# Kernel optimization log

Measured on AMD Instinct MI355X. Metric: run time of the kernel, lower is better.

Reference implementation:

```python
import jax, jax.numpy as jnp
import numpy as np

B, T, F = 512, 1024, 32
LAYER_SIZES = [64, 32]


def _lstm_layer(x_seq, h0, c0, Wih, Whh, bih, bhh):
    """Single-layer LSTM, batch_first x_seq [B,T,in]. PyTorch gate order i,f,g,o."""
    # Precompute input contribution for all timesteps: [B,T,4H]
    xg = jnp.einsum('bti,gi->btg', x_seq, Wih) + bih + bhh

    def step(carry, xg_t):
        h, c = carry
        gates = xg_t + h @ Whh.T  # [B,4H]
        i, f, g, o = jnp.split(gates, 4, axis=-1)
        i = jax.nn.sigmoid(i)
        f = jax.nn.sigmoid(f)
        g = jnp.tanh(g)
        o = jax.nn.sigmoid(o)
        c = f * c + i * g
        h = o * jnp.tanh(c)
        return (h, c), h

    (hT, cT), hs = jax.lax.scan(step, (h0, c0), jnp.swapaxes(xg, 0, 1))
    return jnp.swapaxes(hs, 0, 1), hT, cT  # [B,T,H], [B,H], [B,H]


def setup_inputs() -> dict:
    key = jax.random.key(0)
    ks = jax.random.split(key, 16)
    x = jax.random.normal(ks[0], (B, T, F), dtype=jnp.float32)
    inp = {'x': x}
    in_size = F
    ki = 1
    for li, h in enumerate(LAYER_SIZES):
        scale_ih = 1.0 / np.sqrt(in_size)
        scale_hh = 1.0 / np.sqrt(h)
        inp[f'W_ih{li}'] = jax.random.normal(ks[ki], (4 * h, in_size), dtype=jnp.float32) * scale_ih; ki += 1
        inp[f'W_hh{li}'] = jax.random.normal(ks[ki], (4 * h, h), dtype=jnp.float32) * scale_hh; ki += 1
        inp[f'b_ih{li}'] = jnp.zeros((4 * h,), dtype=jnp.float32)
        inp[f'b_hh{li}'] = jnp.zeros((4 * h,), dtype=jnp.float32)
        in_size = h
    inp['fc_w'] = jax.random.normal(ks[ki], (1, LAYER_SIZES[-1]), dtype=jnp.float32) * (1.0 / np.sqrt(LAYER_SIZES[-1]))
    inp['fc_b'] = jnp.zeros((1,), dtype=jnp.float32)
    return inp


def reference(x, W_ih0, W_hh0, b_ih0, b_hh0, W_ih1, W_hh1, b_ih1, b_hh1, fc_w, fc_b):
    batch = x.shape[0]
    h0 = jnp.zeros((batch, LAYER_SIZES[0]), dtype=x.dtype)
    c0 = jnp.zeros((batch, LAYER_SIZES[0]), dtype=x.dtype)
    h1 = jnp.zeros((batch, LAYER_SIZES[1]), dtype=x.dtype)
    c1 = jnp.zeros((batch, LAYER_SIZES[1]), dtype=x.dtype)

    out0, hT0, cT0 = _lstm_layer(x, h0, c0, W_ih0, W_hh0, b_ih0, b_hh0)
    # dropout_prob = 0.0 -> identity between layers
    out1, hT1, cT1 = _lstm_layer(out0, h1, c1, W_ih1, W_hh1, b_ih1, b_hh1)

    out = out1[:, -1, :] @ fc_w.T + fc_b  # [B,1]
    # apply_clipped_relu = False -> identity final activation
    return out, hT0, cT0, hT1, cT1
```

## Files before the change

kernel.cpp:

```cpp
#include <hip/hip_runtime.h>

#define B_ 512
#define T_ 1024
#define F_ 32
#define H0_ 64
#define H1_ 32
#define ROWS 2
#define NT 512
#define CH 64
#define NCH (T_ / CH)

typedef _Float16 f16x8 __attribute__((ext_vector_type(8)));
typedef _Float16 f16x4 __attribute__((ext_vector_type(4)));
typedef float f32x4 __attribute__((ext_vector_type(4)));

__device__ __forceinline__ float exp2_f(float x) { return __builtin_amdgcn_exp2f(x); }

__device__ __forceinline__ f16x8 cvt8(const float* p) {
    float4 a = *(const float4*)p;
    float4 b = *(const float4*)(p + 4);
    f16x8 o;
    o[0] = (_Float16)a.x; o[1] = (_Float16)a.y; o[2] = (_Float16)a.z; o[3] = (_Float16)a.w;
    o[4] = (_Float16)b.x; o[5] = (_Float16)b.y; o[6] = (_Float16)b.z; o[7] = (_Float16)b.w;
    return o;
}
__device__ __forceinline__ f16x4 cvt4(float4 v) {
    f16x4 o;
    o[0] = (_Float16)v.x; o[1] = (_Float16)v.y; o[2] = (_Float16)v.z; o[3] = (_Float16)v.w;
    return o;
}

#define K_SIG (-1.4426950408889634f)
#define K_TNH (-2.8853900817779268f)

__global__ void __launch_bounds__(NT, 1) lstm2_mfma_kernel(
    const float* __restrict__ x,
    const float* __restrict__ Wih0, const float* __restrict__ Whh0,
    const float* __restrict__ bih0, const float* __restrict__ bhh0,
    const float* __restrict__ Wih1, const float* __restrict__ Whh1,
    const float* __restrict__ bih1, const float* __restrict__ bhh1,
    const float* __restrict__ fcw, const float* __restrict__ fcb,
    float* __restrict__ out)
{
    __shared__ __align__(16) _Float16 xch[2][CH][ROWS][F_];
    __shared__ __align__(16) _Float16 h0b[2][ROWS][H0_];
    __shared__ __align__(16) _Float16 h1b[2][ROWS][H1_];
    __shared__ __align__(16) float wscr[6][128];
    __shared__ float h1fin[ROWS][H1_];

    const int tid = threadIdx.x, blk = blockIdx.x;
    const int wv = tid >> 6, lane = tid & 63;
    const int lrow = lane & 15;
    const int lk   = lane >> 4;
    const bool isL0 = (wv < 4);
    const bool isL1 = (wv == 4 || wv == 5);
    const int U0 = isL0 ? 16 * wv : 16 * (wv - 4);

    f16x8 aw[4][3];
    if (isL0) {
#pragma unroll
        for (int G = 0; G < 4; ++G) {
            const int r = G * H0_ + U0 + lrow;
            aw[G][0] = cvt8(&Wih0[r * F_ + 8 * lk]);
            aw[G][1] = cvt8(&Whh0[r * H0_ + 8 * lk]);
            aw[G][2] = cvt8(&Whh0[r * H0_ + 32 + 8 * lk]);
        }
    } else if (isL1) {
#pragma unroll
        for (int G = 0; G < 4; ++G) {
            const int r = G * H1_ + U0 + lrow;
            aw[G][0] = cvt8(&Wih1[r * H0_ + 8 * lk]);
            aw[G][1] = cvt8(&Wih1[r * H0_ + 32 + 8 * lk]);
            aw[G][2] = cvt8(&Whh1[r * H1_ + 8 * lk]);
        }
    }

    const float kS1 = (lane < 32) ? K_TNH : K_SIG;
    const float kA1 = (lane < 32) ? 2.0f : 1.0f;
    const float kC1 = (lane < 32) ? -1.0f : 0.0f;
    float bK0 = 0.0f, bK1 = 0.0f;
    if (isL0) {
        const int r0 = (lane >> 5) * H0_ + U0 + (lane & 15);
        const int r1 = (2 + (lane >> 5)) * H0_ + U0 + (lane & 15);
        bK0 = (bih0[r0] + bhh0[r0]) * K_SIG;
        bK1 = (bih0[r1] + bhh0[r1]) * kS1;
    } else if (isL1) {
        const int r0 = (lane >> 5) * H1_ + U0 + (lane & 15);
        const int r1 = (2 + (lane >> 5)) * H1_ + U0 + (lane & 15);
        bK0 = (bih1[r0] + bhh1[r0]) * K_SIG;
        bK1 = (bih1[r1] + bhh1[r1]) * kS1;
    }

    {
        const float4* x4 = (const float4*)x;
#pragma unroll
        for (int k = 0; k < 2; ++k) {
            const int i = tid + k * NT;
            const int b = i >> 9, rem = i & 511;
            const int s2 = rem >> 3, f4 = rem & 7;
            float4 v = x4[(size_t)(2 * blk + b) * (T_ * (F_ / 4)) + s2 * (F_ / 4) + f4];
            *(f16x4*)&xch[0][s2][b][f4 * 4] = cvt4(v);
        }
    }
    if (tid < 256) ((_Float16*)h0b)[tid] = (_Float16)0.0f;
    if (tid < 128) ((_Float16*)h1b)[tid] = (_Float16)0.0f;
    __syncthreads();

    int p = 0, cb = 0;
    float c = 0.0f, hreg = 0.0f;
    for (int it = 0; it <= T_; ++it) {
        const int s = it & (CH - 1);
        const bool active = (isL0 && it < T_) || (isL1 && it >= 1);
        if (active) {
            f16x8 b0, b1, b2;
            if (isL0) {
                b0 = *(const f16x8*)&xch[cb][s][lane & 1][8 * lk];
                b1 = *(const f16x8*)&h0b[p][lane & 1][8 * lk];
                b2 = *(const f16x8*)&h0b[p][lane & 1][32 + 8 * lk];
            } else {
                b0 = *(const f16x8*)&h0b[p][lane & 1][8 * lk];
                b1 = *(const f16x8*)&h0b[p][lane & 1][32 + 8 * lk];
                b2 = *(const f16x8*)&h1b[p][lane & 1][8 * lk];
            }
            f32x4 acc[4];
#pragma unroll
            for (int G = 0; G < 4; ++G) {
                f32x4 a = {0.f, 0.f, 0.f, 0.f};
                a = __builtin_amdgcn_mfma_f32_16x16x32_f16(aw[G][0], b0, a, 0, 0, 0);
                a = __builtin_amdgcn_mfma_f32_16x16x32_f16(aw[G][1], b1, a, 0, 0, 0);
                a = __builtin_amdgcn_mfma_f32_16x16x32_f16(aw[G][2], b2, a, 0, 0, 0);
                acc[G] = a;
            }
            if (lrow < 2) {
                float* sp = &wscr[wv][lrow * 16 + lk * 4];
#pragma unroll
                for (int G = 0; G < 4; ++G) {
                    *(float2*)&sp[G * 32]     = make_float2(acc[G][0], acc[G][1]);
                    *(float2*)&sp[G * 32 + 2] = make_float2(acc[G][2], acc[G][3]);
                }
            }
            const float v0 = wscr[wv][lane];
            const float v1 = wscr[wv][64 + lane];
            const float act0 = __builtin_amdgcn_rcpf(1.0f + exp2_f(fmaf(v0, K_SIG, bK0)));
            const float rr1  = __builtin_amdgcn_rcpf(1.0f + exp2_f(fmaf(v1, kS1, bK1)));
            const float act1 = fmaf(kA1, rr1, kC1);
            const float fg = __shfl_xor(act0, 32, 64);
            const float og = __shfl_xor(act1, 32, 64);
            c = fmaf(fg, c, act0 * act1);
            const float thr = __builtin_amdgcn_rcpf(1.0f + exp2_f(c * K_TNH));
            const float thc = fmaf(2.0f, thr, -1.0f);
            hreg = og * thc;
            if (lane < 32) {
                const _Float16 hq = (_Float16)hreg;
                if (isL0) h0b[p ^ 1][lane >> 4][U0 + (lane & 15)] = hq;
                else      h1b[p ^ 1][lane >> 4][U0 + (lane & 15)] = hq;
            }
        }
        if (wv >= 6) {
            if (s == 0 && (it >> 6) < (NCH - 1)) {
                const int tbase = it + CH;
                const float4* x4 = (const float4*)x;
                const int ls = tid - 384;
#pragma unroll
                for (int k = 0; k < 8; ++k) {
                    const int i = ls + k * 128;
                    const int b = i >> 9, rem = i & 511;
                    const int s2 = rem >> 3, f4 = rem & 7;
                    float4 v = x4[(size_t)(2 * blk + b) * (T_ * (F_ / 4)) + (tbase + s2) * (F_ / 4) + f4];
                    *(f16x4*)&xch[cb ^ 1][s2][b][f4 * 4] = cvt4(v);
                }
            }
        }
        __syncthreads();
        p ^= 1;
        if (s == CH - 1) cb ^= 1;
    }

    float* hT0 = out + B_;
    float* cT0 = hT0 + B_ * H0_;
    float* hT1 = cT0 + B_ * H0_;
    float* cT1 = hT1 + B_ * H1_;
    if (isL0 && lane < 32) {
        const int row = 2 * blk + (lane >> 4), unit = U0 + (lane & 15);
        hT0[row * H0_ + unit] = hreg;
        cT0[row * H0_ + unit] = c;
    }
    if (isL1 && lane < 32) {
        const int row = 2 * blk + (lane >> 4), unit = U0 + (lane & 15);
        hT1[row * H1_ + unit] = hreg;
        cT1[row * H1_ + unit] = c;
        h1fin[lane >> 4][unit] = hreg;
    }
    __syncthreads();
    if (wv == 0) {
        const int u = lane & 31, r = lane >> 5;
        float v = h1fin[r][u] * fcw[u];
        v += __shfl_xor(v, 16, 64);
        v += __shfl_xor(v, 8, 64);
        v += __shfl_xor(v, 4, 64);
        v += __shfl_xor(v, 2, 64);
        v += __shfl_xor(v, 1, 64);
        if (u == 0) out[2 * blk + r] = v + fcb[0];
    }
}

extern "C" void kernel_launch(void* const* d_in, const int* in_sizes, int n_in,
                              void* d_out, int out_size, void* d_ws, size_t ws_size,
                              hipStream_t stream) {
    const float* x    = (const float*)d_in[0];
    const float* Wih0 = (const float*)d_in[1];
    const float* Whh0 = (const float*)d_in[2];
    const float* bih0 = (const float*)d_in[3];
    const float* bhh0 = (const float*)d_in[4];
    const float* Wih1 = (const float*)d_in[5];
    const float* Whh1 = (const float*)d_in[6];
    const float* bih1 = (const float*)d_in[7];
    const float* bhh1 = (const float*)d_in[8];
    const float* fcw  = (const float*)d_in[9];
    const float* fcb  = (const float*)d_in[10];

    hipLaunchKernelGGL(lstm2_mfma_kernel, dim3(B_ / ROWS), dim3(NT), 0, stream,
                       x, Wih0, Whh0, bih0, bhh0, Wih1, Whh1, bih1, bhh1,
                       fcw, fcb, (float*)d_out);
}
```

Measured before the change: 683.2 us.

## Swap MFMA operands so gate outputs land in registers, drop LDS scratch

Swaps the A/B operands of the MFMA so each lane holds the pre-activations for its hidden unit across both batch rows directly in accumulator registers. The LSTM cell update then runs entirely in registers, removing the LDS scratch round-trip (wscr writes and reads) and the cross-lane shuffles on the serial per-step critical path. In exchange, each lane computes 10 transcendental activations instead of 5, only 16 lanes do useful work, and the code relies on the accumulator element layout matching batch rows.

```diff
diff --git a/kernel.cpp b/kernel.cpp
--- a/kernel.cpp
+++ b/kernel.cpp
@@ -15,6 +15,7 @@
 typedef float f32x4 __attribute__((ext_vector_type(4)));
 
 __device__ __forceinline__ float exp2_f(float x) { return __builtin_amdgcn_exp2f(x); }
+__device__ __forceinline__ float rcp_f(float x) { return __builtin_amdgcn_rcpf(x); }
 
 __device__ __forceinline__ f16x8 cvt8(const float* p) {
     float4 a = *(const float4*)p;
@@ -45,7 +46,6 @@
     __shared__ __align__(16) _Float16 xch[2][CH][ROWS][F_];
     __shared__ __align__(16) _Float16 h0b[2][ROWS][H0_];
     __shared__ __align__(16) _Float16 h1b[2][ROWS][H1_];
-    __shared__ __align__(16) float wscr[6][128];
     __shared__ float h1fin[ROWS][H1_];
 
     const int tid = threadIdx.x, blk = blockIdx.x;
@@ -75,20 +75,19 @@
         }
     }
 
-    const float kS1 = (lane < 32) ? K_TNH : K_SIG;
-    const float kA1 = (lane < 32) ? 2.0f : 1.0f;
-    const float kC1 = (lane < 32) ? -1.0f : 0.0f;
-    float bK0 = 0.0f, bK1 = 0.0f;
+    float bK[4] = {0.f, 0.f, 0.f, 0.f};
     if (isL0) {
-        const int r0 = (lane >> 5) * H0_ + U0 + (lane & 15);
-        const int r1 = (2 + (lane >> 5)) * H0_ + U0 + (lane & 15);
-        bK0 = (bih0[r0] + bhh0[r0]) * K_SIG;
-        bK1 = (bih0[r1] + bhh0[r1]) * kS1;
+#pragma unroll
+        for (int G = 0; G < 4; ++G) {
+            const int r = G * H0_ + U0 + lrow;
+            bK[G] = (bih0[r] + bhh0[r]) * ((G == 2) ? K_TNH : K_SIG);
+        }
     } else if (isL1) {
-        const int r0 = (lane >> 5) * H1_ + U0 + (lane & 15);
-        const int r1 = (2 + (lane >> 5)) * H1_ + U0 + (lane & 15);
-        bK0 = (bih1[r0] + bhh1[r0]) * K_SIG;
-        bK1 = (bih1[r1] + bhh1[r1]) * kS1;
+#pragma unroll
+        for (int G = 0; G < 4; ++G) {
+            const int r = G * H1_ + U0 + lrow;
+            bK[G] = (bih1[r] + bhh1[r]) * ((G == 2) ? K_TNH : K_SIG);
+        }
     }
 
     {
@@ -107,7 +106,8 @@
     __syncthreads();
 
     int p = 0, cb = 0;
-    float c = 0.0f, hreg = 0.0f;
+    float cc[2] = {0.f, 0.f};
+    float hh[2] = {0.f, 0.f};
     for (int it = 0; it <= T_; ++it) {
         const int s = it & (CH - 1);
         const bool active = (isL0 && it < T_) || (isL1 && it >= 1);
@@ -126,34 +126,29 @@
 #pragma unroll
             for (int G = 0; G < 4; ++G) {
                 f32x4 a = {0.f, 0.f, 0.f, 0.f};
-                a = __builtin_amdgcn_mfma_f32_16x16x32_f16(aw[G][0], b0, a, 0, 0, 0);
-                a = __builtin_amdgcn_mfma_f32_16x16x32_f16(aw[G][1], b1, a, 0, 0, 0);
-                a = __builtin_amdgcn_mfma_f32_16x16x32_f16(aw[G][2], b2, a, 0, 0, 0);
+                a = __builtin_amdgcn_mfma_f32_16x16x32_f16(b0, aw[G][0], a, 0, 0, 0);
+                a = __builtin_amdgcn_mfma_f32_16x16x32_f16(b1, aw[G][1], a, 0, 0, 0);
+                a = __builtin_amdgcn_mfma_f32_16x16x32_f16(b2, aw[G][2], a, 0, 0, 0);
                 acc[G] = a;
             }
-            if (lrow < 2) {
-                float* sp = &wscr[wv][lrow * 16 + lk * 4];
-#pragma unroll
-                for (int G = 0; G < 4; ++G) {
-                    *(float2*)&sp[G * 32]     = make_float2(acc[G][0], acc[G][1]);
-                    *(float2*)&sp[G * 32 + 2] = make_float2(acc[G][2], acc[G][3]);
+#pragma unroll
+            for (int r = 0; r < 2; ++r) {
+                const float gi = rcp_f(1.0f + exp2_f(fmaf(acc[0][r], K_SIG, bK[0])));
+                const float gf = rcp_f(1.0f + exp2_f(fmaf(acc[1][r], K_SIG, bK[1])));
+                const float gg = fmaf(2.0f, rcp_f(1.0f + exp2_f(fmaf(acc[2][r], K_TNH, bK[2]))), -1.0f);
+                const float go = rcp_f(1.0f + exp2_f(fmaf(acc[3][r], K_SIG, bK[3])));
+                cc[r] = fmaf(gf, cc[r], gi * gg);
+                const float th = fmaf(2.0f, rcp_f(1.0f + exp2_f(cc[r] * K_TNH)), -1.0f);
+                hh[r] = go * th;
+            }
+            if (lane < 16) {
+                if (isL0) {
+                    h0b[p ^ 1][0][U0 + lane] = (_Float16)hh[0];
+                    h0b[p ^ 1][1][U0 + lane] = (_Float16)hh[1];
+                } else {
+                    h1b[p ^ 1][0][U0 + lane] = (_Float16)hh[0];
+                    h1b[p ^ 1][1][U0 + lane] = (_Float16)hh[1];
                 }
-            }
-            const float v0 = wscr[wv][lane];
-            const float v1 = wscr[wv][64 + lane];
-            const float act0 = __builtin_amdgcn_rcpf(1.0f + exp2_f(fmaf(v0, K_SIG, bK0)));
-            const float rr1  = __builtin_amdgcn_rcpf(1.0f + exp2_f(fmaf(v1, kS1, bK1)));
-            const float act1 = fmaf(kA1, rr1, kC1);
-            const float fg = __shfl_xor(act0, 32, 64);
-            const float og = __shfl_xor(act1, 32, 64);
-            c = fmaf(fg, c, act0 * act1);
-            const float thr = __builtin_amdgcn_rcpf(1.0f + exp2_f(c * K_TNH));
-            const float thc = fmaf(2.0f, thr, -1.0f);
-            hreg = og * thc;
-            if (lane < 32) {
-                const _Float16 hq = (_Float16)hreg;
-                if (isL0) h0b[p ^ 1][lane >> 4][U0 + (lane & 15)] = hq;
-                else      h1b[p ^ 1][lane >> 4][U0 + (lane & 15)] = hq;
             }
         }
         if (wv >= 6) {
@@ -180,16 +175,22 @@
     float* cT0 = hT0 + B_ * H0_;
     float* hT1 = cT0 + B_ * H0_;
     float* cT1 = hT1 + B_ * H1_;
-    if (isL0 && lane < 32) {
-        const int row = 2 * blk + (lane >> 4), unit = U0 + (lane & 15);
-        hT0[row * H0_ + unit] = hreg;
-        cT0[row * H0_ + unit] = c;
-    }
-    if (isL1 && lane < 32) {
-        const int row = 2 * blk + (lane >> 4), unit = U0 + (lane & 15);
-        hT1[row * H1_ + unit] = hreg;
-        cT1[row * H1_ + unit] = c;
-        h1fin[lane >> 4][unit] = hreg;
+    if (lane < 16) {
+        const int unit = U0 + lane;
+        if (isL0) {
+#pragma unroll
+            for (int b = 0; b < 2; ++b) {
+                hT0[(2 * blk + b) * H0_ + unit] = hh[b];
+                cT0[(2 * blk + b) * H0_ + unit] = cc[b];
+            }
+        } else if (isL1) {
+#pragma unroll
+            for (int b = 0; b < 2; ++b) {
+                hT1[(2 * blk + b) * H1_ + unit] = hh[b];
+                cT1[(2 * blk + b) * H1_ + unit] = cc[b];
+                h1fin[b][unit] = hh[b];
+            }
+        }
     }
     __syncthreads();
     if (wv == 0) {
```

Measured after the change: 721.6 us. +5.6%, slower.
